# Kernel optimization log

Measured on AMD Instinct MI355X. Metric: run time of the kernel, lower is better.

Reference implementation:

```python
import jax, jax.numpy as jnp
import numpy as np

N_NODES = 50000
N_EDGES = 800000
IN_FEATS = 256
OUT_FEATS = 128


def setup_inputs() -> dict:
    key = jax.random.key(0)
    k1, k2, k3, k4 = jax.random.split(key, 4)
    feat = jax.random.normal(k1, (N_NODES, IN_FEATS), dtype=jnp.float32)
    # xavier uniform init for weight [in, out]
    limit = float(np.sqrt(6.0 / (IN_FEATS + OUT_FEATS)))
    weight = jax.random.uniform(k2, (IN_FEATS, OUT_FEATS), minval=-limit, maxval=limit, dtype=jnp.float32)
    bias = jnp.zeros((OUT_FEATS,), dtype=jnp.float32)
    src = jax.random.randint(k3, (N_EDGES,), 0, N_NODES, dtype=jnp.int32)
    dst = jax.random.randint(k4, (N_EDGES,), 0, N_NODES, dtype=jnp.int32)
    return {"feat": feat, "weight": weight, "bias": bias, "src": src, "dst": dst}


def reference(feat, weight, bias, src, dst):
    N = feat.shape[0]
    in_f, out_f = weight.shape
    # right normalization: 1 / out_degree(src node), clamped to >= 1
    deg = jax.ops.segment_sum(jnp.ones(src.shape[0], dtype=feat.dtype), src, num_segments=N)
    norm = (1.0 / jnp.maximum(deg, 1.0))[:, None]  # [N,1]
    if in_f > out_f:
        # transform first (cheaper messages), then normalize + aggregate
        h = jnp.matmul(feat, weight) * norm          # [N, out]
        rst = jax.ops.segment_sum(h[src], dst, num_segments=N)  # scatter-sum over edges
    else:
        h = feat * norm                               # [N, in]
        rst = jax.ops.segment_sum(h[src], dst, num_segments=N)
        rst = jnp.matmul(rst, weight)
    return rst + bias
```

## Files before the change

kernel.cpp:

```cpp
#include <hip/hip_runtime.h>

#define N_NODES 50000
#define N_EDGES 800000
#define IN_F 256
#define OUT_F 128

#define CHUNKS 128
#define EPC (N_EDGES / CHUNKS)
#define BINW (N_NODES / 4)
#define NWORDS (N_NODES / 4)
#define RGB 196
#define HIST_BLOCKS (2 * CHUNKS)
#define CPW (CHUNKS / 4)

#define GEMMF_BLOCKS 196
#define SCATF_BLOCKS 391

typedef __attribute__((ext_vector_type(8))) short short8;
typedef __attribute__((ext_vector_type(4))) float float4_t;

__device__ __forceinline__ short f2bf(float f) {
  unsigned u = __builtin_bit_cast(unsigned, f);
  u = u + 0x7FFFu + ((u >> 16) & 1u);
  return (short)(u >> 16);
}

__device__ __forceinline__ float bflo(unsigned u) {
  return __builtin_bit_cast(float, u << 16);
}
__device__ __forceinline__ float bfhi(unsigned u) {
  return __builtin_bit_cast(float, u & 0xFFFF0000u);
}

__global__ __launch_bounds__(512) void hist_kernel(const int* __restrict__ src,
                                                   const int* __restrict__ dst,
                                                   unsigned char* __restrict__ pdst8,
                                                   unsigned char* __restrict__ psrc8,
                                                   unsigned char* __restrict__ rank8,
                                                   int* __restrict__ cursor) {
  __shared__ unsigned bins[BINW];
  int b = blockIdx.x;
  int tid = threadIdx.x;
  if (b == 0 && tid == 0) *cursor = 0;
  int hs = b >> 7;
  int c = b & 127;
  uint4* b4 = (uint4*)bins;
  for (int j = tid; j < BINW / 4; j += 512) b4[j] = (uint4){0u, 0u, 0u, 0u};
  __syncthreads();
  const int* key = hs ? src : dst;
  int e0 = c * EPC;

  auto process = [&](int v, int eI) {
    unsigned sh = (v & 3) * 8;
    unsigned old = atomicAdd(&bins[v >> 2], 1u << sh);
    if (!hs) rank8[eI] = (unsigned char)((old >> sh) & 0xFFu);
  };

#pragma unroll 2
  for (int tile = 0; tile < 3; ++tile) {
    int i = tile * 2048 + tid;
    int k0 = key[e0 + i];
    int k1 = key[e0 + i + 512];
    int k2 = key[e0 + i + 1024];
    int k3 = key[e0 + i + 1536];
    process(k0, e0 + i);
    process(k1, e0 + i + 512);
    process(k2, e0 + i + 1024);
    process(k3, e0 + i + 1536);
  }
  {
    int i = 6144 + tid;
    if (i < EPC) process(key[e0 + i], e0 + i);
  }
  __syncthreads();
  uint4* p128 = (uint4*)((hs ? psrc8 : pdst8) + (size_t)c * N_NODES);
  const uint4* s128 = (const uint4*)bins;
  for (int j = tid; j < BINW / 4; j += 512) p128[j] = s128[j];
}

__global__ __launch_bounds__(256) void reduceoff_kernel(const unsigned char* __restrict__ pdst8,
                                                        const unsigned char* __restrict__ psrc8,
                                                        unsigned char* __restrict__ delta8,
                                                        int* __restrict__ cnt,
                                                        int* __restrict__ row_start,
                                                        int* __restrict__ cursor,
                                                        float* __restrict__ norm) {
  __shared__ unsigned tot[4][64];
  int g = blockIdx.x, side = blockIdx.y;
  int t = threadIdx.x;
  int w = t >> 6, l = t & 63;
  int wd = g * 64 + l;
  bool ok = wd < NWORDS;
  int wdc = ok ? wd : NWORDS - 1;
  const unsigned* P = (const unsigned*)(side == 0 ? pdst8 : psrc8);

  unsigned vals[CPW];
  unsigned s = 0;
#pragma unroll
  for (int i = 0; i < CPW; ++i) {
    vals[i] = P[(size_t)(w * CPW + i) * NWORDS + wdc];
    s += vals[i];
  }
  tot[w][l] = s;
  __syncthreads();

  if (side == 0) {
    unsigned base = 0;
#pragma unroll
    for (int w2 = 0; w2 < 4; ++w2)
      if (w2 < w) base += tot[w2][l];
    unsigned run = base;
    unsigned* D = (unsigned*)delta8;
    if (ok) {
#pragma unroll
      for (int i = 0; i < CPW; ++i) {
        D[(size_t)(w * CPW + i) * NWORDS + wd] = run;
        run += vals[i];
      }
    }
    if (w == 0) {
      unsigned ftot = tot[0][l] + tot[1][l] + tot[2][l] + tot[3][l];
      if (!ok) ftot = 0;
      int c0 = ftot & 255, c1 = (ftot >> 8) & 255, c2 = (ftot >> 16) & 255, c3 = ftot >> 24;
      int T = c0 + c1 + c2 + c3;
      int x = T;
#pragma unroll
      for (int off = 1; off < 64; off <<= 1) {
        int y = __shfl_up(x, off);
        if (l >= off) x += y;
      }
      int waveTotal = __shfl(x, 63);
      int sb = 0;
      if (l == 63) sb = atomicAdd(cursor, waveTotal);
      sb = __shfl(sb, 63);
      int E = sb + x - T;
      if (ok) {
        int4 cv = {c0, c1, c2, c3};
        int4 rv = {E, E + c0, E + c0 + c1, E + c0 + c1 + c2};
        ((int4*)cnt)[wd] = cv;
        ((int4*)row_start)[wd] = rv;
      }
    }
  } else {
    if (w == 0 && ok) {
      unsigned ftot = tot[0][l] + tot[1][l] + tot[2][l] + tot[3][l];
      float4 nv;
      int d0 = ftot & 255, d1 = (ftot >> 8) & 255, d2 = (ftot >> 16) & 255, d3 = (int)(ftot >> 24);
      nv.x = 1.0f / (float)(d0 > 1 ? d0 : 1);
      nv.y = 1.0f / (float)(d1 > 1 ? d1 : 1);
      nv.z = 1.0f / (float)(d2 > 1 ? d2 : 1);
      nv.w = 1.0f / (float)(d3 > 1 ? d3 : 1);
      ((float4*)norm)[wd] = nv;
    }
  }
}

__global__ __launch_bounds__(512) void sg_kernel(const float* __restrict__ feat,
                                                 const float* __restrict__ W,
                                                 unsigned short* __restrict__ h,
                                                 const int* __restrict__ src,
                                                 const int* __restrict__ dst,
                                                 const int* __restrict__ row_start,
                                                 const unsigned char* __restrict__ delta8,
                                                 const unsigned char* __restrict__ rank8,
                                                 int* __restrict__ eidx) {
  __shared__ uint4 smem4[4096];
  int b = blockIdx.x;
  int tid = threadIdx.x;

  if (b < GEMMF_BLOCKS) {
    short* wl = (short*)smem4;
#pragma unroll
    for (int i = 0; i < 64; ++i) {
      int idx = i * 512 + tid;
      int k = idx >> 7, n = idx & 127;
      int s = k >> 5, q = (k >> 3) & 3, j = k & 7;
      int tt = n >> 4, m = n & 15;
      wl[((s * 8 + tt) * 64 + q * 16 + m) * 8 + j] = f2bf(W[idx]);
    }
    __syncthreads();

    int w = tid >> 6, l = tid & 63;
    int m = l & 15, q = l >> 4;
    long base = (long)b * 256 + w * 32;

    float4_t acc[2][8];
#pragma unroll
    for (int r = 0; r < 2; ++r)
#pragma unroll
      for (int to = 0; to < 8; ++to) acc[r][to] = (float4_t)(0.0f);

    long row0 = base + m;
    long row1 = base + 16 + m;
    long r0c = row0 < N_NODES - 1 ? row0 : N_NODES - 1;
    long r1c = row1 < N_NODES - 1 ? row1 : N_NODES - 1;
    const float* a0p = feat + (size_t)r0c * IN_F;
    const float* a1p = feat + (size_t)r1c * IN_F;
    const short8* wl8 = (const short8*)smem4;

#pragma unroll
    for (int s = 0; s < 8; ++s) {
      int k0 = s * 32 + q * 8;
      float4_t av0a = *(const float4_t*)(a0p + k0);
      float4_t av0b = *(const float4_t*)(a0p + k0 + 4);
      float4_t av1a = *(const float4_t*)(a1p + k0);
      float4_t av1b = *(const float4_t*)(a1p + k0 + 4);
      short8 fa0, fa1;
#pragma unroll
      for (int i = 0; i < 4; ++i) {
        fa0[i] = f2bf(av0a[i]);
        fa0[i + 4] = f2bf(av0b[i]);
        fa1[i] = f2bf(av1a[i]);
        fa1[i + 4] = f2bf(av1b[i]);
      }
#pragma unroll
      for (int to = 0; to < 8; ++to) {
        short8 fb = wl8[(s * 8 + to) * 64 + l];
        acc[0][to] = __builtin_amdgcn_mfma_f32_16x16x32_bf16(fa0, fb, acc[0][to], 0, 0, 0);
        acc[1][to] = __builtin_amdgcn_mfma_f32_16x16x32_bf16(fa1, fb, acc[1][to], 0, 0, 0);
      }
    }

#pragma unroll
    for (int r = 0; r < 2; ++r) {
#pragma unroll
      for (int i = 0; i < 4; ++i) {
        long row = base + r * 16 + q * 4 + i;
        if (row < N_NODES) {
          size_t ho = (size_t)row * OUT_F;
#pragma unroll
          for (int to = 0; to < 8; ++to) {
            h[ho + to * 16 + m] = (unsigned short)f2bf(acc[r][to][i]);
          }
        }
      }
    }
    return;
  }

  int sb = b - GEMMF_BLOCKS;
  int gt = sb * 512 + tid;
  int e = gt * 4;
  if (e >= N_EDGES) return;
  int4 d4 = *(const int4*)(dst + e);
  int4 s4 = *(const int4*)(src + e);
  unsigned rr = *(const unsigned*)(rank8 + e);
  int dd[4] = {d4.x, d4.y, d4.z, d4.w};
  int ss[4] = {s4.x, s4.y, s4.z, s4.w};
#pragma unroll
  for (int k = 0; k < 4; ++k) {
    int c = (e + k) / EPC;
    int d = dd[k];
    int pos = row_start[d] + (int)delta8[(size_t)c * N_NODES + d] + (int)((rr >> (8 * k)) & 0xFFu);
    eidx[pos] = ss[k];
  }
}

__global__ __launch_bounds__(256) void agg_kernel(const unsigned short* __restrict__ h,
                                                  const int* __restrict__ row_start,
                                                  const int* __restrict__ cnt,
                                                  const int* __restrict__ eidx,
                                                  const float* __restrict__ norm,
                                                  const float* __restrict__ bias,
                                                  float* __restrict__ out) {
  int w = threadIdx.x >> 6, l = threadIdx.x & 63;
  int d = blockIdx.x * 4 + w;
  int rs = row_start[d], re = rs + cnt[d];
  const uint4* __restrict__ hu4 = (const uint4*)h;
  int rowsel = l >> 4;
  int cp = l & 15;
  float a0 = 0.f, a1 = 0.f, a2 = 0.f, a3 = 0.f, a4 = 0.f, a5 = 0.f, a6 = 0.f, a7 = 0.f;

  auto acc8 = [&](uint4 v, float nm) {
    a0 = fmaf(bflo(v.x), nm, a0); a1 = fmaf(bfhi(v.x), nm, a1);
    a2 = fmaf(bflo(v.y), nm, a2); a3 = fmaf(bfhi(v.y), nm, a3);
    a4 = fmaf(bflo(v.z), nm, a4); a5 = fmaf(bfhi(v.z), nm, a5);
    a6 = fmaf(bflo(v.w), nm, a6); a7 = fmaf(bfhi(v.w), nm, a7);
  };

  for (int bse = rs; bse < re; bse += 64) {
    int n = re - bse; if (n > 64) n = 64;
    int e = (l < n) ? eidx[bse + l] : 0;
    int quarter = (n + 3) >> 2;
    int j = 0;
    for (; j + 4 <= quarter; j += 4) {
      int i0 = 4 * j + rowsel;
      int s0 = __shfl(e, i0);
      int s1 = __shfl(e, i0 + 4);
      int s2 = __shfl(e, i0 + 8);
      int s3 = __shfl(e, i0 + 12);
      uint4 v0 = hu4[(size_t)s0 * 16 + cp];
      uint4 v1 = hu4[(size_t)s1 * 16 + cp];
      uint4 v2 = hu4[(size_t)s2 * 16 + cp];
      uint4 v3 = hu4[(size_t)s3 * 16 + cp];
      float nm0 = norm[s0], nm1 = norm[s1], nm2 = norm[s2], nm3 = norm[s3];
      if (i0 >= n) v0 = (uint4){0u, 0u, 0u, 0u};
      if (i0 + 4 >= n) v1 = (uint4){0u, 0u, 0u, 0u};
      if (i0 + 8 >= n) v2 = (uint4){0u, 0u, 0u, 0u};
      if (i0 + 12 >= n) v3 = (uint4){0u, 0u, 0u, 0u};
      acc8(v0, nm0);
      acc8(v1, nm1);
      acc8(v2, nm2);
      acc8(v3, nm3);
    }
    for (; j < quarter; ++j) {
      int i0 = 4 * j + rowsel;
      int s0 = __shfl(e, i0);
      uint4 v0 = hu4[(size_t)s0 * 16 + cp];
      float nm0 = norm[s0];
      if (i0 >= n) v0 = (uint4){0u, 0u, 0u, 0u};
      acc8(v0, nm0);
    }
  }
  a0 += __shfl_xor(a0, 16); a1 += __shfl_xor(a1, 16);
  a2 += __shfl_xor(a2, 16); a3 += __shfl_xor(a3, 16);
  a4 += __shfl_xor(a4, 16); a5 += __shfl_xor(a5, 16);
  a6 += __shfl_xor(a6, 16); a7 += __shfl_xor(a7, 16);
  a0 += __shfl_xor(a0, 32); a1 += __shfl_xor(a1, 32);
  a2 += __shfl_xor(a2, 32); a3 += __shfl_xor(a3, 32);
  a4 += __shfl_xor(a4, 32); a5 += __shfl_xor(a5, 32);
  a6 += __shfl_xor(a6, 32); a7 += __shfl_xor(a7, 32);
  if (rowsel == 0) {
    float4 b0 = ((const float4*)bias)[2 * cp];
    float4 b1 = ((const float4*)bias)[2 * cp + 1];
    float4 o0, o1;
    o0.x = a0 + b0.x; o0.y = a1 + b0.y; o0.z = a2 + b0.z; o0.w = a3 + b0.w;
    o1.x = a4 + b1.x; o1.y = a5 + b1.y; o1.z = a6 + b1.z; o1.w = a7 + b1.w;
    float4* op = (float4*)(out + (size_t)d * OUT_F + 8 * cp);
    op[0] = o0;
    op[1] = o1;
  }
}

extern "C" void kernel_launch(void* const* d_in, const int* in_sizes, int n_in,
                              void* d_out, int out_size, void* d_ws, size_t ws_size,
                              hipStream_t stream) {
  const float* feat = (const float*)d_in[0];
  const float* weight = (const float*)d_in[1];
  const float* bias = (const float*)d_in[2];
  const int* src = (const int*)d_in[3];
  const int* dst = (const int*)d_in[4];
  float* out = (float*)d_out;

  char* ws = (char*)d_ws;
  size_t off = 0;
  auto alloc = [&](size_t bytes) -> void* {
    void* p = ws + off;
    off += (bytes + 511) & ~(size_t)511;
    return p;
  };
  int* cursor = (int*)alloc(4);
  int* cnt = (int*)alloc(N_NODES * 4);
  int* row_start = (int*)alloc(N_NODES * 4);
  float* norm = (float*)alloc(N_NODES * 4);
  int* eidx = (int*)alloc(N_EDGES * 4);
  unsigned short* h = (unsigned short*)alloc((size_t)N_NODES * OUT_F * 2);
  unsigned char* pdst8 = (unsigned char*)alloc((size_t)CHUNKS * N_NODES);
  unsigned char* psrc8 = (unsigned char*)alloc((size_t)CHUNKS * N_NODES);
  unsigned char* delta8 = (unsigned char*)alloc((size_t)CHUNKS * N_NODES);
  unsigned char* rank8 = (unsigned char*)alloc((size_t)N_EDGES);
  (void)off; (void)ws_size; (void)in_sizes; (void)n_in; (void)out_size;

  hipLaunchKernelGGL(hist_kernel, dim3(HIST_BLOCKS), dim3(512), 0, stream,
                     src, dst, pdst8, psrc8, rank8, cursor);
  hipLaunchKernelGGL(reduceoff_kernel, dim3(RGB, 2), dim3(256), 0, stream,
                     pdst8, psrc8, delta8, cnt, row_start, cursor, norm);
  hipLaunchKernelGGL(sg_kernel, dim3(GEMMF_BLOCKS + SCATF_BLOCKS), dim3(512), 0, stream,
                     feat, weight, h, src, dst, row_start, delta8, rank8, eidx);
  hipLaunchKernelGGL(agg_kernel, dim3(N_NODES / 4), dim3(256), 0, stream,
                     h, row_start, cnt, eidx, norm, bias, out);
}
```

Before: 171.4 us.

## Fuse GEMM with degree reduction kernel and split edge scatter into own kernel

Moves the dense GEMM blocks out of the scatter kernel and co-launches them with the prefix/degree reduction blocks, so the GEMM overlaps the reduction instead of the scatter. The reduction now uses 512-thread blocks with 8 waves each handling 16 chunks. The edge scatter becomes a standalone 256-thread kernel. The launch count stays the same. The overlap now happens in a different stage, and the reduction blocks share LDS sizing with the GEMM.

```diff
diff --git a/kernel.cpp b/kernel.cpp
--- a/kernel.cpp
+++ b/kernel.cpp
@@ -11,10 +11,10 @@
 #define NWORDS (N_NODES / 4)
 #define RGB 196
 #define HIST_BLOCKS (2 * CHUNKS)
-#define CPW (CHUNKS / 4)
+#define CPW8 (CHUNKS / 8)
 
 #define GEMMF_BLOCKS 196
-#define SCATF_BLOCKS 391
+#define SCAT_BLOCKS 782
 
 typedef __attribute__((ext_vector_type(8))) short short8;
 typedef __attribute__((ext_vector_type(4))) float float4_t;
@@ -78,27 +78,105 @@
   for (int j = tid; j < BINW / 4; j += 512) p128[j] = s128[j];
 }
 
-__global__ __launch_bounds__(256) void reduceoff_kernel(const unsigned char* __restrict__ pdst8,
-                                                        const unsigned char* __restrict__ psrc8,
-                                                        unsigned char* __restrict__ delta8,
-                                                        int* __restrict__ cnt,
-                                                        int* __restrict__ row_start,
-                                                        int* __restrict__ cursor,
-                                                        float* __restrict__ norm) {
-  __shared__ unsigned tot[4][64];
-  int g = blockIdx.x, side = blockIdx.y;
-  int t = threadIdx.x;
-  int w = t >> 6, l = t & 63;
+__global__ __launch_bounds__(512) void gemmred_kernel(const float* __restrict__ feat,
+                                                      const float* __restrict__ W,
+                                                      unsigned short* __restrict__ h,
+                                                      const unsigned char* __restrict__ pdst8,
+                                                      const unsigned char* __restrict__ psrc8,
+                                                      unsigned char* __restrict__ delta8,
+                                                      int* __restrict__ cnt,
+                                                      int* __restrict__ row_start,
+                                                      int* __restrict__ cursor,
+                                                      float* __restrict__ norm) {
+  __shared__ uint4 smem4[4096];
+  int b = blockIdx.x;
+  int tid = threadIdx.x;
+
+  if (b < GEMMF_BLOCKS) {
+    short* wl = (short*)smem4;
+#pragma unroll
+    for (int i = 0; i < 64; ++i) {
+      int idx = i * 512 + tid;
+      int k = idx >> 7, n = idx & 127;
+      int s = k >> 5, q = (k >> 3) & 3, j = k & 7;
+      int tt = n >> 4, m = n & 15;
+      wl[((s * 8 + tt) * 64 + q * 16 + m) * 8 + j] = f2bf(W[idx]);
+    }
+    __syncthreads();
+
+    int w = tid >> 6, l = tid & 63;
+    int m = l & 15, q = l >> 4;
+    long base = (long)b * 256 + w * 32;
+
+    float4_t acc[2][8];
+#pragma unroll
+    for (int r = 0; r < 2; ++r)
+#pragma unroll
+      for (int to = 0; to < 8; ++to) acc[r][to] = (float4_t)(0.0f);
+
+    long row0 = base + m;
+    long row1 = base + 16 + m;
+    long r0c = row0 < N_NODES - 1 ? row0 : N_NODES - 1;
+    long r1c = row1 < N_NODES - 1 ? row1 : N_NODES - 1;
+    const float* a0p = feat + (size_t)r0c * IN_F;
+    const float* a1p = feat + (size_t)r1c * IN_F;
+    const short8* wl8 = (const short8*)smem4;
+
+#pragma unroll
+    for (int s = 0; s < 8; ++s) {
+      int k0 = s * 32 + q * 8;
+      float4_t av0a = *(const float4_t*)(a0p + k0);
+      float4_t av0b = *(const float4_t*)(a0p + k0 + 4);
+      float4_t av1a = *(const float4_t*)(a1p + k0);
+      float4_t av1b = *(const float4_t*)(a1p + k0 + 4);
+      short8 fa0, fa1;
+#pragma unroll
+      for (int i = 0; i < 4; ++i) {
+        fa0[i] = f2bf(av0a[i]);
+        fa0[i + 4] = f2bf(av0b[i]);
+        fa1[i] = f2bf(av1a[i]);
+        fa1[i + 4] = f2bf(av1b[i]);
+      }
+#pragma unroll
+      for (int to = 0; to < 8; ++to) {
+        short8 fb = wl8[(s * 8 + to) * 64 + l];
+        acc[0][to] = __builtin_amdgcn_mfma_f32_16x16x32_bf16(fa0, fb, acc[0][to], 0, 0, 0);
+        acc[1][to] = __builtin_amdgcn_mfma_f32_16x16x32_bf16(fa1, fb, acc[1][to], 0, 0, 0);
+      }
+    }
+
+#pragma unroll
+    for (int r = 0; r < 2; ++r) {
+#pragma unroll
+      for (int i = 0; i < 4; ++i) {
+        long row = base + r * 16 + q * 4 + i;
+        if (row < N_NODES) {
+          size_t ho = (size_t)row * OUT_F;
+#pragma unroll
+          for (int to = 0; to < 8; ++to) {
+            h[ho + to * 16 + m] = (unsigned short)f2bf(acc[r][to][i]);
+          }
+        }
+      }
+    }
+    return;
+  }
+
+  int rb = b - GEMMF_BLOCKS;
+  int side = rb >= RGB ? 1 : 0;
+  int g = rb - side * RGB;
+  int w = tid >> 6, l = tid & 63;
   int wd = g * 64 + l;
   bool ok = wd < NWORDS;
   int wdc = ok ? wd : NWORDS - 1;
   const unsigned* P = (const unsigned*)(side == 0 ? pdst8 : psrc8);
-
-  unsigned vals[CPW];
+  unsigned(*tot)[64] = (unsigned(*)[64])smem4;
+
+  unsigned vals[CPW8];
   unsigned s = 0;
 #pragma unroll
-  for (int i = 0; i < CPW; ++i) {
-    vals[i] = P[(size_t)(w * CPW + i) * NWORDS + wdc];
+  for (int i = 0; i < CPW8; ++i) {
+    vals[i] = P[(size_t)(w * CPW8 + i) * NWORDS + wdc];
     s += vals[i];
   }
   tot[w][l] = s;
@@ -107,19 +185,21 @@
   if (side == 0) {
     unsigned base = 0;
 #pragma unroll
-    for (int w2 = 0; w2 < 4; ++w2)
+    for (int w2 = 0; w2 < 8; ++w2)
       if (w2 < w) base += tot[w2][l];
     unsigned run = base;
     unsigned* D = (unsigned*)delta8;
     if (ok) {
 #pragma unroll
-      for (int i = 0; i < CPW; ++i) {
-        D[(size_t)(w * CPW + i) * NWORDS + wd] = run;
+      for (int i = 0; i < CPW8; ++i) {
+        D[(size_t)(w * CPW8 + i) * NWORDS + wd] = run;
         run += vals[i];
       }
     }
     if (w == 0) {
-      unsigned ftot = tot[0][l] + tot[1][l] + tot[2][l] + tot[3][l];
+      unsigned ftot = 0;
+#pragma unroll
+      for (int w2 = 0; w2 < 8; ++w2) ftot += tot[w2][l];
       if (!ok) ftot = 0;
       int c0 = ftot & 255, c1 = (ftot >> 8) & 255, c2 = (ftot >> 16) & 255, c3 = ftot >> 24;
       int T = c0 + c1 + c2 + c3;
@@ -143,7 +223,9 @@
     }
   } else {
     if (w == 0 && ok) {
-      unsigned ftot = tot[0][l] + tot[1][l] + tot[2][l] + tot[3][l];
+      unsigned ftot = 0;
+#pragma unroll
+      for (int w2 = 0; w2 < 8; ++w2) ftot += tot[w2][l];
       float4 nv;
       int d0 = ftot & 255, d1 = (ftot >> 8) & 255, d2 = (ftot >> 16) & 255, d3 = (int)(ftot >> 24);
       nv.x = 1.0f / (float)(d0 > 1 ? d0 : 1);
@@ -155,91 +237,13 @@
   }
 }
 
-__global__ __launch_bounds__(512) void sg_kernel(const float* __restrict__ feat,
-                                                 const float* __restrict__ W,
-                                                 unsigned short* __restrict__ h,
-                                                 const int* __restrict__ src,
-                                                 const int* __restrict__ dst,
-                                                 const int* __restrict__ row_start,
-                                                 const unsigned char* __restrict__ delta8,
-                                                 const unsigned char* __restrict__ rank8,
-                                                 int* __restrict__ eidx) {
-  __shared__ uint4 smem4[4096];
-  int b = blockIdx.x;
-  int tid = threadIdx.x;
-
-  if (b < GEMMF_BLOCKS) {
-    short* wl = (short*)smem4;
-#pragma unroll
-    for (int i = 0; i < 64; ++i) {
-      int idx = i * 512 + tid;
-      int k = idx >> 7, n = idx & 127;
-      int s = k >> 5, q = (k >> 3) & 3, j = k & 7;
-      int tt = n >> 4, m = n & 15;
-      wl[((s * 8 + tt) * 64 + q * 16 + m) * 8 + j] = f2bf(W[idx]);
-    }
-    __syncthreads();
-
-    int w = tid >> 6, l = tid & 63;
-    int m = l & 15, q = l >> 4;
-    long base = (long)b * 256 + w * 32;
-
-    float4_t acc[2][8];
-#pragma unroll
-    for (int r = 0; r < 2; ++r)
-#pragma unroll
-      for (int to = 0; to < 8; ++to) acc[r][to] = (float4_t)(0.0f);
-
-    long row0 = base + m;
-    long row1 = base + 16 + m;
-    long r0c = row0 < N_NODES - 1 ? row0 : N_NODES - 1;
-    long r1c = row1 < N_NODES - 1 ? row1 : N_NODES - 1;
-    const float* a0p = feat + (size_t)r0c * IN_F;
-    const float* a1p = feat + (size_t)r1c * IN_F;
-    const short8* wl8 = (const short8*)smem4;
-
-#pragma unroll
-    for (int s = 0; s < 8; ++s) {
-      int k0 = s * 32 + q * 8;
-      float4_t av0a = *(const float4_t*)(a0p + k0);
-      float4_t av0b = *(const float4_t*)(a0p + k0 + 4);
-      float4_t av1a = *(const float4_t*)(a1p + k0);
-      float4_t av1b = *(const float4_t*)(a1p + k0 + 4);
-      short8 fa0, fa1;
-#pragma unroll
-      for (int i = 0; i < 4; ++i) {
-        fa0[i] = f2bf(av0a[i]);
-        fa0[i + 4] = f2bf(av0b[i]);
-        fa1[i] = f2bf(av1a[i]);
-        fa1[i + 4] = f2bf(av1b[i]);
-      }
-#pragma unroll
-      for (int to = 0; to < 8; ++to) {
-        short8 fb = wl8[(s * 8 + to) * 64 + l];
-        acc[0][to] = __builtin_amdgcn_mfma_f32_16x16x32_bf16(fa0, fb, acc[0][to], 0, 0, 0);
-        acc[1][to] = __builtin_amdgcn_mfma_f32_16x16x32_bf16(fa1, fb, acc[1][to], 0, 0, 0);
-      }
-    }
-
-#pragma unroll
-    for (int r = 0; r < 2; ++r) {
-#pragma unroll
-      for (int i = 0; i < 4; ++i) {
-        long row = base + r * 16 + q * 4 + i;
-        if (row < N_NODES) {
-          size_t ho = (size_t)row * OUT_F;
-#pragma unroll
-          for (int to = 0; to < 8; ++to) {
-            h[ho + to * 16 + m] = (unsigned short)f2bf(acc[r][to][i]);
-          }
-        }
-      }
-    }
-    return;
-  }
-
-  int sb = b - GEMMF_BLOCKS;
-  int gt = sb * 512 + tid;
+__global__ __launch_bounds__(256) void scat_kernel(const int* __restrict__ src,
+                                                   const int* __restrict__ dst,
+                                                   const int* __restrict__ row_start,
+                                                   const unsigned char* __restrict__ delta8,
+                                                   const unsigned char* __restrict__ rank8,
+                                                   int* __restrict__ eidx) {
+  int gt = blockIdx.x * 256 + threadIdx.x;
   int e = gt * 4;
   if (e >= N_EDGES) return;
   int4 d4 = *(const int4*)(dst + e);
@@ -363,10 +367,10 @@
 
   hipLaunchKernelGGL(hist_kernel, dim3(HIST_BLOCKS), dim3(512), 0, stream,
                      src, dst, pdst8, psrc8, rank8, cursor);
-  hipLaunchKernelGGL(reduceoff_kernel, dim3(RGB, 2), dim3(256), 0, stream,
-                     pdst8, psrc8, delta8, cnt, row_start, cursor, norm);
-  hipLaunchKernelGGL(sg_kernel, dim3(GEMMF_BLOCKS + SCATF_BLOCKS), dim3(512), 0, stream,
-                     feat, weight, h, src, dst, row_start, delta8, rank8, eidx);
+  hipLaunchKernelGGL(gemmred_kernel, dim3(GEMMF_BLOCKS + 2 * RGB), dim3(512), 0, stream,
+                     feat, weight, h, pdst8, psrc8, delta8, cnt, row_start, cursor, norm);
+  hipLaunchKernelGGL(scat_kernel, dim3(SCAT_BLOCKS), dim3(256), 0, stream,
+                     src, dst, row_start, delta8, rank8, eidx);
   hipLaunchKernelGGL(agg_kernel, dim3(N_NODES / 4), dim3(256), 0, stream,
                      h, row_start, cnt, eidx, norm, bias, out);
 }
```

Result: faster. 166.6 us (-2.8%).
